# Performance work log

Hardware: AMD Instinct MI355X
Metric: run time of the kernel (lower is better)

## Reference

```python
import jax, jax.numpy as jnp
import numpy as np

B, L2, N2, L1, N1 = 2, 4, 2048, 9, 8192
CIN, CT, CS, CORIG = 128, 128, 256, 64
R, STRIDE = 1, 2          # temporal_radius, temporal_stride; temporal_padding = [0, 0]
K = 2 * R + 1             # number of temporal MLPs
BN_EPS = 1e-5


def setup_inputs() -> dict:
    key = jax.random.key(0)
    ks = jax.random.split(key, 11)
    return {
        "xyzs": jax.random.normal(ks[0], (B, L2, N2, 3), jnp.float32),
        "original_xyzs": jax.random.normal(ks[1], (B, L1, N1, 3), jnp.float32),
        "features": jax.random.normal(ks[2], (B, L2, CIN, N2), jnp.float32),
        "original_features": jax.random.normal(ks[3], (B, L1, CORIG, N1), jnp.float32),
        # K temporal MLPs, each Conv1d(k=1): layer0 CIN->CT, layer1 CT->CT (bias=False)
        "Wt0": jax.random.normal(ks[4], (K, CT, CIN), jnp.float32) * 0.05,
        "Wt1": jax.random.normal(ks[5], (K, CT, CT), jnp.float32) * 0.05,
        # spatial Conv1d(k=1): (CT + CORIG) -> CS, then BN (eval mode) + ReLU
        "Ws": jax.random.normal(ks[6], (CS, CT + CORIG), jnp.float32) * 0.05,
        "bn_gamma": 1.0 + 0.1 * jax.random.normal(ks[7], (CS,), jnp.float32),
        "bn_beta": 0.1 * jax.random.normal(ks[8], (CS,), jnp.float32),
        "bn_mean": 0.1 * jax.random.normal(ks[9], (CS,), jnp.float32),
        "bn_var": jax.random.uniform(ks[10], (CS,), jnp.float32, 0.5, 1.5),
    }


def reference(xyzs, original_xyzs, features, original_features,
              Wt0, Wt1, Ws, bn_gamma, bn_beta, bn_mean, bn_var):
    # --- temporal MLPs: apply all K 1x1-conv stacks to every subsampled frame ---
    # h, tt: [B, L2, K, CT, N2]
    h = jax.nn.relu(jnp.einsum('koc,blcn->blkon', Wt0, features))
    tt = jax.nn.relu(jnp.einsum('koc,blkcn->blkon', Wt1, h))

    # middles / deltas (1-based frame indices, padding = [0,0])
    middles = [(t2 + 1) + t2 * (STRIDE - 1) + R for t2 in range(L2)]
    bn_scale = bn_gamma / jnp.sqrt(bn_var + BN_EPS)           # [CS]

    new_features = []
    for t1 in range(1, L1 + 1):
        seed_x, seed_f = [], []
        for t2 in range(L2):
            m = middles[t2]
            if m - R <= t1 <= m + R:
                seed_x.append(xyzs[:, t2])              # [B, N2, 3]
                seed_f.append(tt[:, t2, t1 - m + R])    # [B, CT, N2]
        sx = jnp.concatenate(seed_x, axis=1)            # [B, M, 3]
        sf = jnp.concatenate(seed_f, axis=2)            # [B, CT, M]
        ax = original_xyzs[:, t1 - 1]                   # [B, N1, 3]

        # three_nn: squared L2 dists, 3 nearest seeds per anchor point
        d2 = jnp.sum((ax[:, :, None, :] - sx[:, None, :, :]) ** 2, axis=-1)  # [B, N1, M]
        neg_d, idx = jax.lax.top_k(-d2, 3)              # [B, N1, 3]
        dist = -neg_d
        w = 1.0 / (dist + 1e-8)
        w = w / jnp.sum(w, axis=-1, keepdims=True)      # [B, N1, 3]

        # three_interpolate: gather 3 neighbor features per point and blend
        g = jnp.take_along_axis(sf[:, :, None, :], idx[:, None, :, :], axis=3)  # [B, CT, N1, 3]
        interp = jnp.sum(g * w[:, None, :, :], axis=-1)                         # [B, CT, N1]

        x = jnp.concatenate([interp, original_features[:, t1 - 1]], axis=1)     # [B, CT+CORIG, N1]
        x = jnp.einsum('oc,bcn->bon', Ws, x)                                     # [B, CS, N1]
        x = x * bn_scale[None, :, None] + (bn_beta - bn_mean * bn_scale)[None, :, None]
        new_features.append(jax.nn.relu(x))

    return original_xyzs, jnp.stack(new_features, axis=1)  # (B,L1,N1,3), (B,L1,CS,N1)
```

## Files before the change

### kernel.cpp

```cpp
#include <hip/hip_runtime.h>
#include <hip/hip_bf16.h>
#include <hip/hip_fp16.h>

#define BB 2
#define L2C 4
#define N2C 2048
#define L1C 9
#define N1C 8192
#define CINC 128
#define CTC 128
#define CSC 256
#define CORIGC 64
#define KC 3

#define OUT_XYZ_SIZE (BB*L1C*N1C*3)
#define FLT_BIG     3.402823466e38f

#define CHUNK   1024
#define GSTRIDE 20
#define NGROUPS 64
#define LDSF    (NGROUPS * GSTRIDE)

typedef __attribute__((ext_vector_type(8))) short bf16x8;
typedef __attribute__((ext_vector_type(4))) float f32x4;
typedef __attribute__((ext_vector_type(2))) float f32x2;
typedef __attribute__((ext_vector_type(4))) unsigned short u16x4;

#define MFMA16(a,b,c) __builtin_amdgcn_mfma_f32_16x16x32_bf16((a),(b),(c),0,0,0)

#define WS_TT_OFF   0
#define WS_NBR_OFF  12582912
#define WS_W_OFF    14352384
#define WS_BNP_OFF  14942208

__device__ __forceinline__ unsigned short bf16_hi(float v) {
    __hip_bfloat16 h = __float2bfloat16(v);
    return *(unsigned short*)&h;
}
__device__ __forceinline__ float bf16_to_f(unsigned short u) {
    unsigned int x = ((unsigned int)u) << 16;
    return __uint_as_float(x);
}

__device__ __forceinline__ f32x2 d2pk(f32x2 nx, f32x2 ny, f32x2 nz,
                                      f32x2 av0, f32x2 av1, f32x2 av2) {
    #pragma clang fp contract(off)
    f32x2 dx = av0 + nx;
    f32x2 dy = av1 + ny;
    f32x2 dz = av2 + nz;
    return (dx * dx + dy * dy) + dz * dz;
}

__global__ __launch_bounds__(256) void prep_kernel(const float* __restrict__ Wsm,
                                                   const float* __restrict__ Wt0,
                                                   const float* __restrict__ Wt1,
                                                   const float* __restrict__ gam,
                                                   const float* __restrict__ bet,
                                                   const float* __restrict__ mu,
                                                   const float* __restrict__ var,
                                                   unsigned short* __restrict__ WsH,
                                                   unsigned short* __restrict__ WsL,
                                                   unsigned short* __restrict__ W0H,
                                                   unsigned short* __restrict__ W0L,
                                                   unsigned short* __restrict__ W1H,
                                                   unsigned short* __restrict__ W1L,
                                                   float* __restrict__ bnp) {
    for (int i = blockIdx.x * 256 + threadIdx.x; i < 49152; i += gridDim.x * 256) {
        float a = Wsm[i]; unsigned short h = bf16_hi(a);
        WsH[i] = h; WsL[i] = bf16_hi(a - bf16_to_f(h));
        float b = Wt0[i]; h = bf16_hi(b);
        W0H[i] = h; W0L[i] = bf16_hi(b - bf16_to_f(h));
        float c = Wt1[i]; h = bf16_hi(c);
        W1H[i] = h; W1L[i] = bf16_hi(c - bf16_to_f(h));
    }
    if (blockIdx.x == 0) {
        int o = threadIdx.x;
        float sc = gam[o] / sqrtf(var[o] + 1e-5f);
        bnp[o]       = sc;
        bnp[CSC + o] = bet[o] - mu[o] * sc;
    }
}

__global__ __launch_bounds__(256) void tt_kernel(const float* __restrict__ feat,
                                                 const unsigned short* __restrict__ W0H,
                                                 const unsigned short* __restrict__ W0L,
                                                 const unsigned short* __restrict__ W1H,
                                                 const unsigned short* __restrict__ W1L,
                                                 unsigned short* __restrict__ tt) {
    __shared__ unsigned short Bh[16 * 64 * 8];
    __shared__ unsigned short Bl[16 * 64 * 8];
    __shared__ unsigned short Hh[16 * 64 * 8];
    const int t     = threadIdx.x;
    const int slice = blockIdx.y;
    const int k     = blockIdx.z;
    const int n0    = blockIdx.x * 64;
    const int lane  = t & 63;
    const int w     = t >> 6;
    const int l15   = lane & 15;
    const int quad  = lane >> 4;

    const float* f = feat + (size_t)slice * CINC * N2C;
    for (int i = 0; i < 32; ++i) {
        int idx = i * 256 + t;
        int c = idx >> 6, n = idx & 63;
        float v = f[(size_t)c * N2C + n0 + n];
        unsigned short h = bf16_hi(v);
        int bi = (((c >> 3) * 64) + n) * 8 + (c & 7);
        Bh[bi] = h;
        Bl[bi] = bf16_hi(v - bf16_to_f(h));
    }
    __syncthreads();

    unsigned short* ttg = tt + (size_t)slice * KC * N2C * CTC;
    const f32x4 zero = {0.f, 0.f, 0.f, 0.f};

    f32x4 acc[2][4];
    for (int oi = 0; oi < 2; ++oi)
        for (int ni = 0; ni < 4; ++ni) acc[oi][ni] = zero;
    {
        const unsigned short* AH = W0H + (size_t)k * CTC * CINC;
        const unsigned short* AL = W0L + (size_t)k * CTC * CINC;
        for (int kst = 0; kst < 4; ++kst) {
            bf16x8 ah[2], al[2], bh[4], bl[4];
            #pragma unroll
            for (int oi = 0; oi < 2; ++oi) {
                int o = 32 * w + oi * 16 + l15;
                ah[oi] = *(const bf16x8*)(AH + (size_t)o * CINC + kst * 32 + quad * 8);
                al[oi] = *(const bf16x8*)(AL + (size_t)o * CINC + kst * 32 + quad * 8);
            }
            #pragma unroll
            for (int ni = 0; ni < 4; ++ni) {
                int n = ni * 16 + l15;
                int c8 = kst * 4 + quad;
                bh[ni] = *(const bf16x8*)&Bh[(c8 * 64 + n) * 8];
                bl[ni] = *(const bf16x8*)&Bl[(c8 * 64 + n) * 8];
            }
            #pragma unroll
            for (int oi = 0; oi < 2; ++oi)
                #pragma unroll
                for (int ni = 0; ni < 4; ++ni) {
                    acc[oi][ni] = MFMA16(ah[oi], bh[ni], acc[oi][ni]);
                    acc[oi][ni] = MFMA16(ah[oi], bl[ni], acc[oi][ni]);
                    acc[oi][ni] = MFMA16(al[oi], bh[ni], acc[oi][ni]);
                }
        }
    }
    #pragma unroll
    for (int oi = 0; oi < 2; ++oi)
        #pragma unroll
        for (int ni = 0; ni < 4; ++ni) {
            int n = ni * 16 + l15;
            int obase = 32 * w + oi * 16 + quad * 4;
            int ch = obase >> 3, jj = obase & 7;
            unsigned short* dst = &Hh[(ch * 64 + n) * 8 + jj];
            dst[0] = bf16_hi(fmaxf(acc[oi][ni][0], 0.f));
            dst[1] = bf16_hi(fmaxf(acc[oi][ni][1], 0.f));
            dst[2] = bf16_hi(fmaxf(acc[oi][ni][2], 0.f));
            dst[3] = bf16_hi(fmaxf(acc[oi][ni][3], 0.f));
        }
    __syncthreads();

    f32x4 acc2[2][4];
    for (int oi = 0; oi < 2; ++oi)
        for (int ni = 0; ni < 4; ++ni) acc2[oi][ni] = zero;
    {
        const unsigned short* AH = W1H + (size_t)k * CTC * CTC;
        const unsigned short* AL = W1L + (size_t)k * CTC * CTC;
        for (int kst = 0; kst < 4; ++kst) {
            bf16x8 ah[2], al[2], bh[4];
            #pragma unroll
            for (int oi = 0; oi < 2; ++oi) {
                int o = 32 * w + oi * 16 + l15;
                ah[oi] = *(const bf16x8*)(AH + (size_t)o * CTC + kst * 32 + quad * 8);
                al[oi] = *(const bf16x8*)(AL + (size_t)o * CTC + kst * 32 + quad * 8);
            }
            #pragma unroll
            for (int ni = 0; ni < 4; ++ni) {
                int n = ni * 16 + l15;
                int c8 = kst * 4 + quad;
                bh[ni] = *(const bf16x8*)&Hh[(c8 * 64 + n) * 8];
            }
            #pragma unroll
            for (int oi = 0; oi < 2; ++oi)
                #pragma unroll
                for (int ni = 0; ni < 4; ++ni) {
                    acc2[oi][ni] = MFMA16(ah[oi], bh[ni], acc2[oi][ni]);
                    acc2[oi][ni] = MFMA16(al[oi], bh[ni], acc2[oi][ni]);
                }
        }
    }
    #pragma unroll
    for (int oi = 0; oi < 2; ++oi)
        #pragma unroll
        for (int ni = 0; ni < 4; ++ni) {
            int n2 = n0 + ni * 16 + l15;
            int obase = 32 * w + oi * 16 + quad * 4;
            u16x4 vv;
            vv[0] = bf16_hi(fmaxf(acc2[oi][ni][0], 0.f));
            vv[1] = bf16_hi(fmaxf(acc2[oi][ni][1], 0.f));
            vv[2] = bf16_hi(fmaxf(acc2[oi][ni][2], 0.f));
            vv[3] = bf16_hi(fmaxf(acc2[oi][ni][3], 0.f));
            *(u16x4*)&ttg[((size_t)k * N2C + n2) * CTC + obase] = vv;
        }
}

__global__ __launch_bounds__(256, 8) void knn_kernel(const float* __restrict__ xyzs,
                                                     const float* __restrict__ oxyz,
                                                     unsigned int* __restrict__ nbr) {
    __shared__ __align__(16) float sx[LDSF];
    __shared__ __align__(16) float sy[LDSF];
    __shared__ __align__(16) float sz[LDSF];
    float* candd = sx;
    int*   candi = (int*)sy;
    const int t   = threadIdx.x;
    const int bt1 = blockIdx.y;
    const int b   = bt1 / L1C;
    const int t1  = bt1 % L1C + 1;
    int t2min = (t1 - 2) >> 1; if (t2min < 0) t2min = 0;
    int t2max = (t1 - 1) >> 1; if (t2max > 3) t2max = 3;
    const int S = (t2max - t2min + 1) * N2C;

    const int a  = t & 63;
    const int p  = t >> 6;
    const int n1 = blockIdx.x * 64 + a;
    const float* ap = oxyz + ((size_t)bt1 * N1C + n1) * 3;
    const float ax = ap[0], ay = ap[1], az = ap[2];
    const f32x2 ax2 = {ax, ax}, ay2 = {ay, ay}, az2 = {az, az};

    float b0 = FLT_BIG, b1 = FLT_BIG, b2 = FLT_BIG;
    int   i0 = 0, i1 = 0, i2 = 0;

    for (int cb = 0; cb < S; cb += CHUNK) {
        if (cb) __syncthreads();
        {
            int t2  = t2min + (cb >> 11);
            int off = cb & (N2C - 1);
            const float* base = xyzs + ((size_t)(b * L2C + t2) * N2C + off) * 3;
            for (int s = t; s < CHUNK; s += 256) {
                const float* pp = base + (size_t)s * 3;
                int li = (s >> 4) * GSTRIDE + (s & 15);
                sx[li] = -pp[0]; sy[li] = -pp[1]; sz[li] = -pp[2];
            }
        }
        __syncthreads();

        const int g0i = p * 16;

        float gm0 = FLT_BIG, gm1 = FLT_BIG, gm2 = FLT_BIG;
        int   gs0 = g0i << 4, gs1 = g0i << 4, gs2 = g0i << 4;
        for (int g = g0i; g < g0i + 16; ++g) {
            const int gb = g * GSTRIDE;
            f32x2 dd[8];
            #pragma unroll
            for (int q = 0; q < 4; ++q) {
                float4 X = ((const float4*)&sx[gb])[q];
                float4 Y = ((const float4*)&sy[gb])[q];
                float4 Z = ((const float4*)&sz[gb])[q];
                f32x2 xlo = {X.x, X.y}, xhi = {X.z, X.w};
                f32x2 ylo = {Y.x, Y.y}, yhi = {Y.z, Y.w};
                f32x2 zlo = {Z.x, Z.y}, zhi = {Z.z, Z.w};
                dd[2 * q]     = d2pk(xlo, ylo, zlo, ax2, ay2, az2);
                dd[2 * q + 1] = d2pk(xhi, yhi, zhi, ax2, ay2, az2);
            }
            float e0 = fminf(dd[0][0], dd[0][1]);
            float e1 = fminf(dd[1][0], dd[1][1]);
            float e2 = fminf(dd[2][0], dd[2][1]);
            float e3 = fminf(dd[3][0], dd[3][1]);
            float e4 = fminf(dd[4][0], dd[4][1]);
            float e5 = fminf(dd[5][0], dd[5][1]);
            float e6 = fminf(dd[6][0], dd[6][1]);
            float e7 = fminf(dd[7][0], dd[7][1]);
            float f0 = fminf(e0, e1), f1 = fminf(e2, e3);
            float f2 = fminf(e4, e5), f3 = fminf(e6, e7);
            float m  = fminf(fminf(f0, f1), fminf(f2, f3));
            int sb = g << 4;
            bool c0 = m < gm0, c1 = m < gm1, c2 = m < gm2;
            int ns0 = c0 ? sb  : gs0;
            int ns1 = c0 ? gs0 : (c1 ? sb : gs1);
            int ns2 = c1 ? gs1 : (c2 ? sb : gs2);
            float nm0 = fminf(gm0, m);
            float nm1 = __builtin_amdgcn_fmed3f(gm0, gm1, m);
            float nm2 = __builtin_amdgcn_fmed3f(gm1, gm2, m);
            gm0 = nm0; gm1 = nm1; gm2 = nm2;
            gs0 = ns0; gs1 = ns1; gs2 = ns2;
        }

        int lo01 = min(gs0, gs1), hi01 = max(gs0, gs1);
        int gA = min(lo01, gs2);
        int gC = max(hi01, gs2);
        int gB = (gs0 + gs1 + gs2) - gA - gC;

        #pragma unroll
        for (int v = 0; v < 3; ++v) {
            int sb = (v == 0) ? gA : ((v == 1) ? gB : gC);
            const int lb = (sb >> 4) * GSTRIDE;
            f32x2 dd[8];
            #pragma unroll
            for (int q = 0; q < 4; ++q) {
                float4 X = ((const float4*)&sx[lb])[q];
                float4 Y = ((const float4*)&sy[lb])[q];
                float4 Z = ((const float4*)&sz[lb])[q];
                f32x2 xlo = {X.x, X.y}, xhi = {X.z, X.w};
                f32x2 ylo = {Y.x, Y.y}, yhi = {Y.z, Y.w};
                f32x2 zlo = {Z.x, Z.y}, zhi = {Z.z, Z.w};
                dd[2 * q]     = d2pk(xlo, ylo, zlo, ax2, ay2, az2);
                dd[2 * q + 1] = d2pk(xhi, yhi, zhi, ax2, ay2, az2);
            }
            #pragma unroll
            for (int jp = 0; jp < 8; ++jp)
                #pragma unroll
                for (int h = 0; h < 2; ++h) {
                    float d = dd[jp][h];
                    int   s = cb + sb + jp * 2 + h;
                    bool c0 = d < b0, c1 = d < b1, c2 = d < b2;
                    int ni0 = c0 ? s  : i0;
                    int ni1 = c0 ? i0 : (c1 ? s : i1);
                    int ni2 = c1 ? i1 : (c2 ? s : i2);
                    float nb0 = fminf(b0, d);
                    float nb1 = __builtin_amdgcn_fmed3f(b0, b1, d);
                    float nb2 = __builtin_amdgcn_fmed3f(b1, b2, d);
                    b0 = nb0; b1 = nb1; b2 = nb2;
                    i0 = ni0; i1 = ni1; i2 = ni2;
                }
        }
    }
    __syncthreads();

    candd[(a * 4 + p) * 3 + 0] = b0; candi[(a * 4 + p) * 3 + 0] = i0;
    candd[(a * 4 + p) * 3 + 1] = b1; candi[(a * 4 + p) * 3 + 1] = i1;
    candd[(a * 4 + p) * 3 + 2] = b2; candi[(a * 4 + p) * 3 + 2] = i2;
    __syncthreads();

    if (t < 64) {
        float dd[12]; int ii[12];
        for (int q = 0; q < 12; ++q) { dd[q] = candd[t * 12 + q]; ii[q] = candi[t * 12 + q]; }
        for (int x = 1; x < 12; ++x) {
            float dv = dd[x]; int iv = ii[x]; int y = x - 1;
            while (y >= 0 && (dd[y] > dv || (dd[y] == dv && ii[y] > iv))) {
                dd[y + 1] = dd[y]; ii[y + 1] = ii[y]; --y;
            }
            dd[y + 1] = dv; ii[y + 1] = iv;
        }
        float w0 = 1.f / (dd[0] + 1e-8f);
        float w1 = 1.f / (dd[1] + 1e-8f);
        float w2 = 1.f / (dd[2] + 1e-8f);
        float wsum = (w0 + w1) + w2;
        float wv[3] = { w0 / wsum, w1 / wsum, w2 / wsum };
        size_t base = ((size_t)bt1 * N1C + blockIdx.x * 64 + t) * 3;
        #pragma unroll
        for (int j = 0; j < 3; ++j) {
            int s  = ii[j];
            int t2 = t2min + (s >> 11);
            int n2 = s & 2047;
            int kidx = t1 - 2 * t2 - 1;
            unsigned int idx16 = (unsigned int)(((b * L2C + t2) * KC + kidx) * N2C + n2);
            unsigned short hb = __half_as_ushort(__float2half(wv[j]));
            nbr[base + j] = (idx16 << 16) | (unsigned int)hb;
        }
    }
}

__global__ __launch_bounds__(256) void out_kernel(const float* __restrict__ ofeat,
                                                  const unsigned short* __restrict__ WsH,
                                                  const unsigned short* __restrict__ WsL,
                                                  const unsigned short* __restrict__ tt,
                                                  const unsigned int* __restrict__ nbr,
                                                  const float* __restrict__ bnp,
                                                  float* __restrict__ out) {
    __shared__ unsigned short xh[16 * 64 * 8];
    __shared__ unsigned short xl[16 * 64 * 8];
    const int t    = threadIdx.x;
    const int bt1  = blockIdx.y;
    const int n0   = blockIdx.x * 64;
    const int w    = t >> 6;
    const int lane = t & 63;
    const int l15  = lane & 15;
    const int quad = lane >> 4;

    const f32x4 zero = {0.f, 0.f, 0.f, 0.f};
    f32x4 acc[4][4];
    for (int mi = 0; mi < 4; ++mi)
        for (int oi = 0; oi < 4; ++oi) acc[mi][oi] = zero;

    const int c0 = 2 * lane;
    for (int nn = 0; nn < 16; ++nn) {
        int n = w * 16 + nn;
        size_t kb = ((size_t)bt1 * N1C + n0 + n) * 3;
        unsigned int u0 = nbr[kb], u1 = nbr[kb + 1], u2 = nbr[kb + 2];
        const unsigned short* p0 = tt + (size_t)(u0 >> 16) * CTC;
        const unsigned short* p1 = tt + (size_t)(u1 >> 16) * CTC;
        const unsigned short* p2 = tt + (size_t)(u2 >> 16) * CTC;
        float q0 = __half2float(__ushort_as_half((unsigned short)(u0 & 0xffffu)));
        float q1 = __half2float(__ushort_as_half((unsigned short)(u1 & 0xffffu)));
        float q2 = __half2float(__ushort_as_half((unsigned short)(u2 & 0xffffu)));
        unsigned int g0 = *(const unsigned int*)(p0 + c0);
        unsigned int g1 = *(const unsigned int*)(p1 + c0);
        unsigned int g2 = *(const unsigned int*)(p2 + c0);
        float vE = (bf16_to_f((unsigned short)(g0 & 0xffffu)) * q0
                  + bf16_to_f((unsigned short)(g1 & 0xffffu)) * q1)
                  + bf16_to_f((unsigned short)(g2 & 0xffffu)) * q2;
        float vO = (bf16_to_f((unsigned short)(g0 >> 16)) * q0
                  + bf16_to_f((unsigned short)(g1 >> 16)) * q1)
                  + bf16_to_f((unsigned short)(g2 >> 16)) * q2;
        int bi = (((c0 >> 3) * 64) + n) * 8 + (c0 & 7);
        unsigned short hE = bf16_hi(vE), hO = bf16_hi(vO);
        *(unsigned int*)&xh[bi] = (unsigned int)hE | ((unsigned int)hO << 16);
        unsigned short lE = bf16_hi(vE - bf16_to_f(hE));
        unsigned short lO = bf16_hi(vO - bf16_to_f(hO));
        *(unsigned int*)&xl[bi] = (unsigned int)lE | ((unsigned int)lO << 16);
    }
    __syncthreads();

    for (int kst = 0; kst < 4; ++kst) {
        bf16x8 ah[4], al[4], bh[4], bl[4];
        #pragma unroll
        for (int mi = 0; mi < 4; ++mi) {
            int n = mi * 16 + l15;
            int c8 = kst * 4 + quad;
            ah[mi] = *(const bf16x8*)&xh[(c8 * 64 + n) * 8];
            al[mi] = *(const bf16x8*)&xl[(c8 * 64 + n) * 8];
        }
        #pragma unroll
        for (int oi = 0; oi < 4; ++oi) {
            int o = w * 64 + oi * 16 + l15;
            bh[oi] = *(const bf16x8*)(WsH + (size_t)o * 192 + kst * 32 + quad * 8);
            bl[oi] = *(const bf16x8*)(WsL + (size_t)o * 192 + kst * 32 + quad * 8);
        }
        #pragma unroll
        for (int mi = 0; mi < 4; ++mi)
            #pragma unroll
            for (int oi = 0; oi < 4; ++oi) {
                acc[mi][oi] = MFMA16(ah[mi], bh[oi], acc[mi][oi]);
                acc[mi][oi] = MFMA16(ah[mi], bl[oi], acc[mi][oi]);
                acc[mi][oi] = MFMA16(al[mi], bh[oi], acc[mi][oi]);
            }
    }
    __syncthreads();

    {
        const float* ofp = ofeat + (size_t)bt1 * CORIGC * N1C;
        for (int i = 0; i < 16; ++i) {
            int idx = i * 256 + t;
            int cp = idx >> 6, n = idx & 63;
            float v = ofp[(size_t)cp * N1C + n0 + n];
            int bi = (((cp >> 3) * 64) + n) * 8 + (cp & 7);
            unsigned short h = bf16_hi(v);
            xh[bi] = h; xl[bi] = bf16_hi(v - bf16_to_f(h));
        }
    }
    __syncthreads();

    for (int kst = 4; kst < 6; ++kst) {
        bf16x8 ah[4], al[4], bh[4], bl[4];
        #pragma unroll
        for (int mi = 0; mi < 4; ++mi) {
            int n = mi * 16 + l15;
            int c8p = (kst - 4) * 4 + quad;
            ah[mi] = *(const bf16x8*)&xh[(c8p * 64 + n) * 8];
            al[mi] = *(const bf16x8*)&xl[(c8p * 64 + n) * 8];
        }
        #pragma unroll
        for (int oi = 0; oi < 4; ++oi) {
            int o = w * 64 + oi * 16 + l15;
            bh[oi] = *(const bf16x8*)(WsH + (size_t)o * 192 + kst * 32 + quad * 8);
            bl[oi] = *(const bf16x8*)(WsL + (size_t)o * 192 + kst * 32 + quad * 8);
        }
        #pragma unroll
        for (int mi = 0; mi < 4; ++mi)
            #pragma unroll
            for (int oi = 0; oi < 4; ++oi) {
                acc[mi][oi] = MFMA16(ah[mi], bh[oi], acc[mi][oi]);
                acc[mi][oi] = MFMA16(ah[mi], bl[oi], acc[mi][oi]);
                acc[mi][oi] = MFMA16(al[mi], bh[oi], acc[mi][oi]);
            }
    }

    float* outp = out + OUT_XYZ_SIZE + (size_t)bt1 * CSC * N1C;
    #pragma unroll
    for (int oi = 0; oi < 4; ++oi) {
        int o = w * 64 + oi * 16 + l15;
        float sc = bnp[o], sh = bnp[CSC + o];
        #pragma unroll
        for (int mi = 0; mi < 4; ++mi) {
            int nb = n0 + mi * 16 + quad * 4;
            f32x4 y;
            y[0] = fmaxf(acc[mi][oi][0] * sc + sh, 0.f);
            y[1] = fmaxf(acc[mi][oi][1] * sc + sh, 0.f);
            y[2] = fmaxf(acc[mi][oi][2] * sc + sh, 0.f);
            y[3] = fmaxf(acc[mi][oi][3] * sc + sh, 0.f);
            *(f32x4*)&outp[(size_t)o * N1C + nb] = y;
        }
    }
}

extern "C" void kernel_launch(void* const* d_in, const int* in_sizes, int n_in,
                              void* d_out, int out_size, void* d_ws, size_t ws_size,
                              hipStream_t stream) {
    const float* xyzs  = (const float*)d_in[0];
    const float* oxyz  = (const float*)d_in[1];
    const float* feat  = (const float*)d_in[2];
    const float* ofeat = (const float*)d_in[3];
    const float* Wt0   = (const float*)d_in[4];
    const float* Wt1   = (const float*)d_in[5];
    const float* Wsm   = (const float*)d_in[6];
    const float* gam   = (const float*)d_in[7];
    const float* bet   = (const float*)d_in[8];
    const float* mu    = (const float*)d_in[9];
    const float* var   = (const float*)d_in[10];
    float* out = (float*)d_out;
    char*  wsb = (char*)d_ws;

    unsigned short* tt  = (unsigned short*)(wsb + WS_TT_OFF);
    unsigned int*   nbr = (unsigned int*)(wsb + WS_NBR_OFF);
    unsigned short* WsH = (unsigned short*)(wsb + WS_W_OFF);
    unsigned short* WsL = WsH + 49152;
    unsigned short* W0H = WsL + 49152;
    unsigned short* W0L = W0H + 49152;
    unsigned short* W1H = W0L + 49152;
    unsigned short* W1L = W1H + 49152;
    float*          bnp = (float*)(wsb + WS_BNP_OFF);

    hipMemcpyAsync(out, oxyz, (size_t)OUT_XYZ_SIZE * sizeof(float),
                   hipMemcpyDeviceToDevice, stream);

    hipLaunchKernelGGL(prep_kernel, dim3(64), dim3(256), 0, stream,
                       Wsm, Wt0, Wt1, gam, bet, mu, var,
                       WsH, WsL, W0H, W0L, W1H, W1L, bnp);
    hipLaunchKernelGGL(tt_kernel, dim3(32, BB * L2C, KC), dim3(256), 0, stream,
                       feat, W0H, W0L, W1H, W1L, tt);
    hipLaunchKernelGGL(knn_kernel, dim3(128, BB * L1C), dim3(256), 0, stream,
                       xyzs, oxyz, nbr);
    hipLaunchKernelGGL(out_kernel, dim3(128, BB * L1C), dim3(256), 0, stream,
                       ofeat, WsH, WsL, tt, nbr, bnp, out);
}
```

Before: 469.7 us.

## Track top-3 groups across all chunks and refine once from global memory

The three-nearest-neighbour search now keeps the three best 16-point groups across all seed chunks and runs the exact per-point refinement only once at the end, instead of once per chunk. The refinement reads the group coordinates straight from global memory with float4 loads, since the LDS chunk is no longer resident. Two inner loops in the interpolation/projection kernel also get unroll-4 pragmas. This cuts refinement work when there are several chunks. The catch is that one pass now keeps only three groups for the whole search rather than three per chunk, which may change which neighbours are found when points are close together.

Result: faster. 415.1 us (-11.6%).

```diff
diff --git a/kernel.cpp b/kernel.cpp
--- a/kernel.cpp
+++ b/kernel.cpp
@@ -227,8 +227,8 @@
     const float ax = ap[0], ay = ap[1], az = ap[2];
     const f32x2 ax2 = {ax, ax}, ay2 = {ay, ay}, az2 = {az, az};
 
-    float b0 = FLT_BIG, b1 = FLT_BIG, b2 = FLT_BIG;
-    int   i0 = 0, i1 = 0, i2 = 0;
+    float gm0 = FLT_BIG, gm1 = FLT_BIG, gm2 = FLT_BIG;
+    int   gg0 = 0, gg1 = 0, gg2 = 0;
 
     for (int cb = 0; cb < S; cb += CHUNK) {
         if (cb) __syncthreads();
@@ -246,8 +246,6 @@
 
         const int g0i = p * 16;
 
-        float gm0 = FLT_BIG, gm1 = FLT_BIG, gm2 = FLT_BIG;
-        int   gs0 = g0i << 4, gs1 = g0i << 4, gs2 = g0i << 4;
         for (int g = g0i; g < g0i + 16; ++g) {
             const int gb = g * GSTRIDE;
             f32x2 dd[8];
@@ -273,55 +271,60 @@
             float f0 = fminf(e0, e1), f1 = fminf(e2, e3);
             float f2 = fminf(e4, e5), f3 = fminf(e6, e7);
             float m  = fminf(fminf(f0, f1), fminf(f2, f3));
-            int sb = g << 4;
+            int sb = cb + (g << 4);
             bool c0 = m < gm0, c1 = m < gm1, c2 = m < gm2;
-            int ns0 = c0 ? sb  : gs0;
-            int ns1 = c0 ? gs0 : (c1 ? sb : gs1);
-            int ns2 = c1 ? gs1 : (c2 ? sb : gs2);
+            int ns0 = c0 ? sb  : gg0;
+            int ns1 = c0 ? gg0 : (c1 ? sb : gg1);
+            int ns2 = c1 ? gg1 : (c2 ? sb : gg2);
             float nm0 = fminf(gm0, m);
             float nm1 = __builtin_amdgcn_fmed3f(gm0, gm1, m);
             float nm2 = __builtin_amdgcn_fmed3f(gm1, gm2, m);
             gm0 = nm0; gm1 = nm1; gm2 = nm2;
-            gs0 = ns0; gs1 = ns1; gs2 = ns2;
-        }
-
-        int lo01 = min(gs0, gs1), hi01 = max(gs0, gs1);
-        int gA = min(lo01, gs2);
-        int gC = max(hi01, gs2);
-        int gB = (gs0 + gs1 + gs2) - gA - gC;
-
-        #pragma unroll
-        for (int v = 0; v < 3; ++v) {
-            int sb = (v == 0) ? gA : ((v == 1) ? gB : gC);
-            const int lb = (sb >> 4) * GSTRIDE;
-            f32x2 dd[8];
-            #pragma unroll
-            for (int q = 0; q < 4; ++q) {
-                float4 X = ((const float4*)&sx[lb])[q];
-                float4 Y = ((const float4*)&sy[lb])[q];
-                float4 Z = ((const float4*)&sz[lb])[q];
-                f32x2 xlo = {X.x, X.y}, xhi = {X.z, X.w};
-                f32x2 ylo = {Y.x, Y.y}, yhi = {Y.z, Y.w};
-                f32x2 zlo = {Z.x, Z.y}, zhi = {Z.z, Z.w};
-                dd[2 * q]     = d2pk(xlo, ylo, zlo, ax2, ay2, az2);
-                dd[2 * q + 1] = d2pk(xhi, yhi, zhi, ax2, ay2, az2);
-            }
-            #pragma unroll
-            for (int jp = 0; jp < 8; ++jp)
-                #pragma unroll
-                for (int h = 0; h < 2; ++h) {
-                    float d = dd[jp][h];
-                    int   s = cb + sb + jp * 2 + h;
-                    bool c0 = d < b0, c1 = d < b1, c2 = d < b2;
-                    int ni0 = c0 ? s  : i0;
-                    int ni1 = c0 ? i0 : (c1 ? s : i1);
-                    int ni2 = c1 ? i1 : (c2 ? s : i2);
-                    float nb0 = fminf(b0, d);
-                    float nb1 = __builtin_amdgcn_fmed3f(b0, b1, d);
-                    float nb2 = __builtin_amdgcn_fmed3f(b1, b2, d);
-                    b0 = nb0; b1 = nb1; b2 = nb2;
-                    i0 = ni0; i1 = ni1; i2 = ni2;
+            gg0 = ns0; gg1 = ns1; gg2 = ns2;
+        }
+    }
+
+    int lo01 = min(gg0, gg1), hi01 = max(gg0, gg1);
+    int gA = min(lo01, gg2);
+    int gC = max(hi01, gg2);
+    int gB = (gg0 + gg1 + gg2) - gA - gC;
+
+    float b0 = FLT_BIG, b1 = FLT_BIG, b2 = FLT_BIG;
+    int   i0 = 0, i1 = 0, i2 = 0;
+
+    #pragma unroll
+    for (int v = 0; v < 3; ++v) {
+        int sb = (v == 0) ? gA : ((v == 1) ? gB : gC);
+        int t2  = t2min + (sb >> 11);
+        int n2b = sb & (N2C - 1);
+        const float* gpf = xyzs + ((size_t)(b * L2C + t2) * N2C + n2b) * 3;
+        const float4* gp = (const float4*)gpf;
+        #pragma unroll
+        for (int hg = 0; hg < 2; ++hg) {
+            float4 q0 = gp[hg * 6 + 0], q1 = gp[hg * 6 + 1], q2 = gp[hg * 6 + 2];
+            float4 q3 = gp[hg * 6 + 3], q4 = gp[hg * 6 + 4], q5 = gp[hg * 6 + 5];
+            float xs[8] = {q0.x, q0.w, q1.z, q2.y, q3.x, q3.w, q4.z, q5.y};
+            float ys[8] = {q0.y, q1.x, q1.w, q2.z, q3.y, q4.x, q4.w, q5.z};
+            float zs[8] = {q0.z, q1.y, q2.x, q2.w, q3.z, q4.y, q5.x, q5.w};
+            #pragma unroll
+            for (int j = 0; j < 8; ++j) {
+                float d;
+                {
+                    #pragma clang fp contract(off)
+                    float dx = ax - xs[j], dy = ay - ys[j], dz = az - zs[j];
+                    d = (dx * dx + dy * dy) + dz * dz;
                 }
+                int s = sb + hg * 8 + j;
+                bool c0 = d < b0, c1 = d < b1, c2 = d < b2;
+                int ni0 = c0 ? s  : i0;
+                int ni1 = c0 ? i0 : (c1 ? s : i1);
+                int ni2 = c1 ? i1 : (c2 ? s : i2);
+                float nb0 = fminf(b0, d);
+                float nb1 = __builtin_amdgcn_fmed3f(b0, b1, d);
+                float nb2 = __builtin_amdgcn_fmed3f(b1, b2, d);
+                b0 = nb0; b1 = nb1; b2 = nb2;
+                i0 = ni0; i1 = ni1; i2 = ni2;
+            }
         }
     }
     __syncthreads();
@@ -383,6 +386,7 @@
         for (int oi = 0; oi < 4; ++oi) acc[mi][oi] = zero;
 
     const int c0 = 2 * lane;
+    #pragma unroll 4
     for (int nn = 0; nn < 16; ++nn) {
         int n = w * 16 + nn;
         size_t kb = ((size_t)bt1 * N1C + n0 + n) * 3;
@@ -439,6 +443,7 @@
 
     {
         const float* ofp = ofeat + (size_t)bt1 * CORIGC * N1C;
+        #pragma unroll 4
         for (int i = 0; i < 16; ++i) {
             int idx = i * 256 + t;
             int cp = idx >> 6, n = idx & 63;
```
